# Performance work log

Measured on AMD Instinct MI355X. Metric: run time of the kernel, lower is better.

Reference implementation:

```python
import jax, jax.numpy as jnp
import numpy as np

EPS = 1e-10


def setup_inputs() -> dict:
    key = jax.random.key(0)
    k1, k2, k3 = jax.random.split(key, 3)
    B, c = 65536, 64
    xyz = jax.random.normal(k1, (B, 3, 1), dtype=jnp.float32)          # group centers
    xyz_group = xyz + 0.1 * jax.random.normal(k2, (B, 3, c), dtype=jnp.float32)  # neighbor points
    r_lrf = 0.2 + 0.8 * jax.random.uniform(k3, (B,), dtype=jnp.float32)  # per-group support radius
    return {"xyz": xyz, "xyz_group": xyz_group, "r_lrf": r_lrf}


def reference(xyz, xyz_group, r_lrf):
    # xyz: [B,3,1] center; xyz_group: [B,3,c] neighbors; r_lrf: [B]
    B, _, c = xyz_group.shape
    x = xyz - xyz_group                                   # [B,3,c]
    xxt = jnp.einsum('bic,bjc->bij', x, x) / c            # [B,3,3] covariance
    _, _, vh = jnp.linalg.svd(xxt)                        # vh: [B,3,3]
    v_last = vh[:, -1, :]                                 # [B,3] smallest singular vector (torch v[...,-1])

    # sign disambiguation (no-grad in the original)
    center_proj = jnp.einsum('bi,bic->bc', v_last, x)     # [B,c]
    sum_ = (center_proj > 0.001).sum(-1) - (center_proj < -0.001).sum(-1)  # [B]
    sign = jax.lax.stop_gradient(1.0 - 2.0 * (sum_ < 0).astype(jnp.float32))  # [B]

    zp = sign[:, None] * v_last                           # [B,3] z axis
    x = -x                                                # x *= -1 in original
    norm = jnp.einsum('bi,bic->bc', zp, x)                # [B,c] projection onto zp
    vi = x - zp[:, :, None] * norm[:, None, :]            # [B,3,c] in-plane component
    x_l2 = jnp.sqrt(jnp.sum(x * x, axis=1))               # [B,c]
    alpha = (r_lrf[:, None] - x_l2) ** 2                  # [B,c]
    beta = norm * norm                                    # [B,c]
    vi_c = jnp.einsum('bc,bic->bi', alpha * beta, vi)     # [B,3] weighted sum
    xp = vi_c / (jnp.sqrt(jnp.sum(vi_c * vi_c, axis=1, keepdims=True)) + EPS)  # [B,3] x axis
    yp = jnp.cross(xp, zp)                                # [B,3] y axis
    lrf = jnp.stack([xp, yp, zp], axis=2)                 # [B,3,3] columns = axes
    out = jnp.einsum('bij,bic->bjc', lrf, (xyz_group - xyz) / r_lrf[:, None, None])  # lrf^T @ _out_xp
    return out


if __name__ == '__main__':
    o = reference(**setup_inputs())
    print(o.shape)
```

## Files before the change

### kernel.cpp

```cpp
#include <hip/hip_runtime.h>


#define DEVFN static __device__ __forceinline__


DEVFN float slapy2f(float x, float y) {
#pragma clang fp contract(off)
  float xa = fabsf(x), ya = fabsf(y);
  float w = fmaxf(xa, ya);
  float z = fminf(xa, ya);
  if (z == 0.0f) return w;
  float q = z / w;
  return w * sqrtf(fmaf(q, q, 1.0f));
}

DEVFN float snrm2_2f(float a, float b) {
  double da = (double)a, db = (double)b;
  return (float)sqrt(da * da + db * db);
}

DEVFN void slartgf(float f, float g, float &cs, float &sn, float &r) {
#pragma clang fp contract(off)
  if (g == 0.0f) { cs = 1.0f; sn = 0.0f; r = f; return; }
  if (f == 0.0f) { cs = 0.0f; sn = copysignf(1.0f, g); r = fabsf(g); return; }
  float f1 = fabsf(f), g1 = fabsf(g);
  const float rtmin = 0x1p-63f;
  const float rtmax = 6.5219089e18f;
  if (f1 > rtmin && f1 < rtmax && g1 > rtmin && g1 < rtmax) {
    float d = sqrtf(fmaf(f, f, g * g));
    cs = f1 / d;
    r = copysignf(d, f);
    sn = g / r;
  } else {
    const float safmin = 0x1p-126f;
    const float safmax = 0x1p+126f;
    float u = fminf(safmax, fmaxf(safmin, fmaxf(f1, g1)));
    float fs = f / u, gs = g / u;
    float d = sqrtf(fmaf(fs, fs, gs * gs));
    cs = fabsf(fs) / d;
    r = copysignf(d, f);
    sn = gs / r;
    r = r * u;
  }
}

DEVFN void slas2f(float f, float g, float h, float &ssmin, float &ssmax) {
#pragma clang fp contract(off)
  float fa = fabsf(f), ga = fabsf(g), ha = fabsf(h);
  float fhmn = fminf(fa, ha), fhmx = fmaxf(fa, ha);
  if (fhmn == 0.0f) {
    ssmin = 0.0f;
    if (fhmx == 0.0f) {
      ssmax = ga;
    } else {
      float mx = fmaxf(fhmx, ga), mn = fminf(fhmx, ga);
      float q = mn / mx;
      ssmax = mx * sqrtf(fmaf(q, q, 1.0f));
    }
  } else {
    if (ga < fhmx) {
      float as = 1.0f + fhmn / fhmx;
      float at = (fhmx - fhmn) / fhmx;
      float qq = ga / fhmx;
      float au = qq * qq;
      float c = 2.0f / (sqrtf(fmaf(as, as, au)) + sqrtf(fmaf(at, at, au)));
      ssmin = fhmn * c;
      ssmax = fhmx / c;
    } else {
      float au = fhmx / ga;
      if (au == 0.0f) {
        ssmin = (fhmn * fhmx) / ga;
        ssmax = ga;
      } else {
        float as = 1.0f + fhmn / fhmx;
        float at = (fhmx - fhmn) / fhmx;
        float q1 = as * au, q2 = at * au;
        float c = 1.0f / (sqrtf(fmaf(q1, q1, 1.0f)) + sqrtf(fmaf(q2, q2, 1.0f)));
        ssmin = (fhmn * c) * au;
        ssmin = ssmin + ssmin;
        ssmax = ga / (c + c);
      }
    }
  }
}

DEVFN void slasv2f(float f, float g, float h, float &ssmin, float &ssmax,
                   float &snr, float &csr, float &snl, float &csl) {
#pragma clang fp contract(off)
  const float eps = 0x1p-24f;
  float ft = f, fa = fabsf(f), ht = h, ha = fabsf(h);
  int pmax = 1;
  bool swp = (ha > fa);
  if (swp) {
    pmax = 3;
    float tmp = ft; ft = ht; ht = tmp;
    tmp = fa; fa = ha; ha = tmp;
  }
  float gt = g, ga = fabsf(g);
  float clt = 0.0f, crt = 0.0f, slt = 0.0f, srt = 0.0f;
  if (ga == 0.0f) {
    ssmin = ha; ssmax = fa;
    clt = 1.0f; crt = 1.0f; slt = 0.0f; srt = 0.0f;
  } else {
    bool gasmal = true;
    if (ga > fa) {
      pmax = 2;
      if ((fa / ga) < eps) {
        gasmal = false;
        ssmax = ga;
        if (ha > 1.0f) ssmin = fa / (ga / ha);
        else ssmin = (fa / ga) * ha;
        clt = 1.0f; slt = ht / gt; srt = 1.0f; crt = ft / gt;
      }
    }
    if (gasmal) {
      float dd = fa - ha;
      float l;
      if (dd == fa) l = 1.0f;
      else l = dd / fa;
      float m = gt / ft;
      float t = 2.0f - l;
      float s = sqrtf(fmaf(m, m, t * t));
      float r;
      if (l == 0.0f) r = fabsf(m);
      else r = sqrtf(fmaf(m, m, l * l));
      float a = 0.5f * (s + r);
      ssmin = ha / a;
      ssmax = fa * a;
      float mm = m * m;
      if (mm == 0.0f) {
        if (l == 0.0f) t = copysignf(2.0f, ft) * copysignf(1.0f, gt);
        else t = gt / copysignf(dd, ft) + m / t;
      } else {
        t = (m / (s + t) + m / (r + l)) * (1.0f + a);
      }
      float l2 = sqrtf(fmaf(t, t, 4.0f));
      crt = 2.0f / l2;
      srt = t / l2;
      clt = fmaf(srt, m, crt) / a;
      slt = (ht / ft) * srt / a;
    }
  }
  if (swp) { csl = srt; snl = crt; csr = slt; snr = clt; }
  else { csl = clt; snl = slt; csr = crt; snr = srt; }
  float tsign = 0.0f;
  if (pmax == 1) tsign = copysignf(1.0f, csr) * copysignf(1.0f, csl) * copysignf(1.0f, f);
  if (pmax == 2) tsign = copysignf(1.0f, snr) * copysignf(1.0f, csl) * copysignf(1.0f, g);
  if (pmax == 3) tsign = copysignf(1.0f, snr) * copysignf(1.0f, snl) * copysignf(1.0f, h);
  ssmax = copysignf(ssmax, tsign);
  ssmin = copysignf(ssmin, tsign * copysignf(1.0f, f) * copysignf(1.0f, h));
}

#define GROT(hi1, hi2, hi3, lo1, lo2, lo3, ct_, st_)          \
  do {                                                        \
    float c__ = (ct_), s__ = (st_);                           \
    if (c__ != 1.0f || s__ != 0.0f) {                         \
      float t_;                                               \
      t_ = hi1; hi1 = fmaf(c__, t_, -(s__ * lo1)); lo1 = fmaf(s__, t_, c__ * lo1); \
      t_ = hi2; hi2 = fmaf(c__, t_, -(s__ * lo2)); lo2 = fmaf(s__, t_, c__ * lo2); \
      t_ = hi3; hi3 = fmaf(c__, t_, -(s__ * lo3)); lo3 = fmaf(s__, t_, c__ * lo3); \
    }                                                         \
  } while (0)

#define ROT2X2(lo1, lo2, lo3, hi1, hi2, hi3, cr_, sr_)        \
  do {                                                        \
    float xx_, yy_, st_;                                      \
    xx_ = lo1; yy_ = hi1; st_ = fmaf(cr_, xx_, sr_ * yy_);    \
    hi1 = fmaf(cr_, yy_, -(sr_ * xx_)); lo1 = st_;            \
    xx_ = lo2; yy_ = hi2; st_ = fmaf(cr_, xx_, sr_ * yy_);    \
    hi2 = fmaf(cr_, yy_, -(sr_ * xx_)); lo2 = st_;            \
    xx_ = lo3; yy_ = hi3; st_ = fmaf(cr_, xx_, sr_ * yy_);    \
    hi3 = fmaf(cr_, yy_, -(sr_ * xx_)); lo3 = st_;            \
  } while (0)

#define VSWAP(a, b) { float t_ = (a); (a) = (b); (b) = t_; }

static __device__ void svd3_vlast(float c00, float c01, float c02,
                                  float c11, float c12, float c22,
                                  float vout[3]) {
#pragma clang fp contract(off)
  float a11 = c00, a12 = c01, a13 = c02;
  float a21 = c01, a22 = c11, a23 = c12;
  float a31 = c02, a32 = c12, a33 = c22;
  float d1, d2, d3, e1, e2;
  float taup1 = 0.0f, g2 = 0.0f;

  {
    float xnorm = snrm2_2f(a21, a31);
    if (xnorm == 0.0f) {
      d1 = a11;
    } else {
      float beta = -copysignf(slapy2f(a11, xnorm), a11);
      float tauq1 = (beta - a11) / beta;
      float sc = 1.0f / (a11 - beta);
      float v2 = a21 * sc, v3 = a31 * sc;
      d1 = beta;
      float w2 = fmaf(a32, v3, a22 * v2);
      float w3 = fmaf(a33, v3, a23 * v2);
      w2 = w2 + a12;
      w3 = w3 + a13;
      a12 = fmaf(-tauq1, w2, a12);
      a13 = fmaf(-tauq1, w3, a13);
      float t2 = -tauq1 * w2;
      float t3 = -tauq1 * w3;
      a22 = fmaf(v2, t2, a22); a32 = fmaf(v3, t2, a32);
      a23 = fmaf(v2, t3, a23); a33 = fmaf(v3, t3, a33);
    }
  }
  {
    float xnorm = fabsf(a13);
    if (xnorm == 0.0f) {
      e1 = a12;
    } else {
      float beta = -copysignf(slapy2f(a12, xnorm), a12);
      taup1 = (beta - a12) / beta;
      g2 = a13 * (1.0f / (a12 - beta));
      e1 = beta;
      float w2 = a23 * g2;
      float w3 = a33 * g2;
      w2 = w2 + a22;
      w3 = w3 + a32;
      a22 = fmaf(-taup1, w2, a22);
      a32 = fmaf(-taup1, w3, a32);
      float tg = -taup1 * g2;
      a23 = fmaf(w2, tg, a23);
      a33 = fmaf(w3, tg, a33);
    }
  }
  {
    float xnorm = fabsf(a32);
    if (xnorm == 0.0f) {
      d2 = a22;
    } else {
      float beta = -copysignf(slapy2f(a22, xnorm), a22);
      float tauq2 = (beta - a22) / beta;
      float h3 = a32 * (1.0f / (a22 - beta));
      d2 = beta;
      float w = a33 * h3;
      w = w + a23;
      a23 = fmaf(-tauq2, w, a23);
      float tw = -tauq2 * w;
      a33 = fmaf(h3, tw, a33);
    }
  }
  e2 = a23;
  d3 = a33;

  float vt11 = 1.0f, vt12 = 0.0f, vt13 = 0.0f;
  float vt21 = 0.0f, vt22 = 1.0f, vt23 = 0.0f;
  float vt31 = 0.0f, vt32 = 0.0f, vt33 = 1.0f;

  const float eps = 0x1p-24f;
  const float unfl = 0x1p-126f;
  const float tol = 10.0f * eps;
  float thresh;
  {
    float sminoa = fabsf(d1);
    if (sminoa != 0.0f) {
      float mu = sminoa;
      mu = fabsf(d2) * (mu / (mu + fabsf(e1)));
      sminoa = fminf(sminoa, mu);
      if (sminoa != 0.0f) {
        mu = fabsf(d3) * (mu / (mu + fabsf(e2)));
        sminoa = fminf(sminoa, mu);
      }
    }
    sminoa = sminoa / sqrtf(3.0f);
    thresh = fmaxf(tol * sminoa, 6.0f * (3.0f * (3.0f * unfl)));
  }
  int mq = 3;
  int iterq = -1, iterdivn = 0;
  const int maxitdivn = 18;
  int oldll = -1, oldm = -1, idir = 0;
  float sminl = 0.0f;
  int guard = 0;

  while (true) {
    if (mq <= 1) break;
    if (++guard > 300) break;
    if (iterq >= 3) {
      iterq -= 3;
      iterdivn += 1;
      if (iterdivn >= maxitdivn) break;
    }
    if (mq == 2) {
      if (fabsf(e1) <= thresh) { e1 = 0.0f; mq = 1; continue; }
      float sigmn, sigmx, sinr, cosr, sinl, cosl;
      slasv2f(d1, e1, d2, sigmn, sigmx, sinr, cosr, sinl, cosl);
      d1 = sigmx; e1 = 0.0f; d2 = sigmn;
      ROT2X2(vt11, vt12, vt13, vt21, vt22, vt23, cosr, sinr);
      mq = 0;
      continue;
    }
    float smax = fabsf(d3);
    if (fabsf(e2) <= thresh) { e2 = 0.0f; mq = 2; continue; }
    smax = fmaxf(fmaxf(smax, fabsf(d2)), fabsf(e2));
    if (fabsf(e1) <= thresh) {
      e1 = 0.0f;
      float sigmn, sigmx, sinr, cosr, sinl, cosl;
      slasv2f(d2, e2, d3, sigmn, sigmx, sinr, cosr, sinl, cosl);
      d2 = sigmx; e2 = 0.0f; d3 = sigmn;
      ROT2X2(vt21, vt22, vt23, vt31, vt32, vt33, cosr, sinr);
      mq = 1;
      continue;
    }
    smax = fmaxf(fmaxf(smax, fabsf(d1)), fabsf(e1));
    if (1 > oldm || 3 < oldll)
      idir = (fabsf(d1) >= fabsf(d3)) ? 1 : 2;
    bool back = false;
    if (idir == 1) {
      if (fabsf(e2) <= tol * fabsf(d3)) { e2 = 0.0f; continue; }
      float mu = fabsf(d1);
      sminl = mu;
      if (fabsf(e1) <= tol * mu) { e1 = 0.0f; back = true; }
      else {
        mu = fabsf(d2) * (mu / (mu + fabsf(e1)));
        sminl = fminf(sminl, mu);
        if (fabsf(e2) <= tol * mu) { e2 = 0.0f; back = true; }
        else {
          mu = fabsf(d3) * (mu / (mu + fabsf(e2)));
          sminl = fminf(sminl, mu);
        }
      }
    } else {
      if (fabsf(e1) <= tol * fabsf(d1)) { e1 = 0.0f; continue; }
      float mu = fabsf(d3);
      sminl = mu;
      if (fabsf(e2) <= tol * mu) { e2 = 0.0f; back = true; }
      else {
        mu = fabsf(d2) * (mu / (mu + fabsf(e2)));
        sminl = fminf(sminl, mu);
        if (fabsf(e1) <= tol * mu) { e1 = 0.0f; back = true; }
        else {
          mu = fabsf(d1) * (mu / (mu + fabsf(e1)));
          sminl = fminf(sminl, mu);
        }
      }
    }
    if (back) continue;
    oldll = 1;
    oldm = 3;
    float shift = 0.0f;
    if (!((3.0f * tol) * (sminl / smax) <= fmaxf(eps, 0.01f * tol))) {
      float sll, rdum;
      if (idir == 1) { sll = fabsf(d1); slas2f(d2, e2, d3, shift, rdum); }
      else { sll = fabsf(d3); slas2f(d1, e1, d2, shift, rdum); }
      if (sll > 0.0f) {
        float q = shift / sll;
        if (q * q < eps) shift = 0.0f;
      }
    }
    iterq += 2;
    float rc0, rc1, rs0, rs1;
    if (shift == 0.0f) {
      if (idir == 1) {
        float cs = 1.0f, oldcs = 1.0f, sn = 0.0f, oldsn = 0.0f, rr = 0.0f;
        float fq = d1 * cs;
        slartgf(fq, e1, cs, sn, rr);
        float f2 = oldcs * rr;
        float g2q = d2 * sn;
        slartgf(f2, g2q, oldcs, oldsn, d1);
        rc0 = cs; rs0 = sn;
        fq = d2 * cs;
        slartgf(fq, e2, cs, sn, rr);
        e1 = oldsn * rr;
        f2 = oldcs * rr;
        g2q = d3 * sn;
        slartgf(f2, g2q, oldcs, oldsn, d2);
        rc1 = cs; rs1 = sn;
        float h = d3 * cs;
        d3 = h * oldcs;
        e2 = h * oldsn;
        GROT(vt21, vt22, vt23, vt11, vt12, vt13, rc0, rs0);
        GROT(vt31, vt32, vt33, vt21, vt22, vt23, rc1, rs1);
        if (fabsf(e2) <= thresh) e2 = 0.0f;
      } else {
        float cs = 1.0f, oldcs = 1.0f, sn = 0.0f, oldsn = 0.0f, rr = 0.0f;
        float fq = d3 * cs;
        slartgf(fq, e2, cs, sn, rr);
        float f2 = oldcs * rr;
        float g2q = d2 * sn;
        slartgf(f2, g2q, oldcs, oldsn, d3);
        rc1 = oldcs; rs1 = -oldsn;
        fq = d2 * cs;
        slartgf(fq, e1, cs, sn, rr);
        e2 = oldsn * rr;
        f2 = oldcs * rr;
        g2q = d1 * sn;
        slartgf(f2, g2q, oldcs, oldsn, d2);
        rc0 = oldcs; rs0 = -oldsn;
        float h = d1 * cs;
        d1 = h * oldcs;
        e1 = h * oldsn;
        GROT(vt31, vt32, vt33, vt21, vt22, vt23, rc1, rs1);
        GROT(vt21, vt22, vt23, vt11, vt12, vt13, rc0, rs0);
        if (fabsf(e1) <= thresh) e1 = 0.0f;
      }
    } else {
      if (idir == 1) {
        float fq = (fabsf(d1) - shift) * (copysignf(1.0f, d1) + shift / d1);
        float gq = e1;
        float cosr = 0, sinr = 0, cosl = 0, sinl = 0, rr = 0;
        slartgf(fq, gq, cosr, sinr, rr);
        fq = fmaf(cosr, d1, sinr * e1);
        e1 = fmaf(cosr, e1, -(sinr * d1));
        gq = sinr * d2;
        d2 = cosr * d2;
        slartgf(fq, gq, cosl, sinl, rr);
        d1 = rr;
        fq = fmaf(cosl, e1, sinl * d2);
        d2 = fmaf(cosl, d2, -(sinl * e1));
        gq = sinl * e2;
        e2 = cosl * e2;
        rc0 = cosr; rs0 = sinr;
        slartgf(fq, gq, cosr, sinr, rr);
        e1 = rr;
        fq = fmaf(cosr, d2, sinr * e2);
        e2 = fmaf(cosr, e2, -(sinr * d2));
        gq = sinr * d3;
        d3 = cosr * d3;
        slartgf(fq, gq, cosl, sinl, rr);
        d2 = rr;
        fq = fmaf(cosl, e2, sinl * d3);
        d3 = fmaf(cosl, d3, -(sinl * e2));
        rc1 = cosr; rs1 = sinr;
        e2 = fq;
        GROT(vt21, vt22, vt23, vt11, vt12, vt13, rc0, rs0);
        GROT(vt31, vt32, vt33, vt21, vt22, vt23, rc1, rs1);
        if (fabsf(e2) <= thresh) e2 = 0.0f;
      } else {
        float fq = (fabsf(d3) - shift) * (copysignf(1.0f, d3) + shift / d3);
        float gq = e2;
        float cosr = 0, sinr = 0, cosl = 0, sinl = 0, rr = 0;
        slartgf(fq, gq, cosr, sinr, rr);
        fq = fmaf(cosr, d3, sinr * e2);
        e2 = fmaf(cosr, e2, -(sinr * d3));
        gq = sinr * d2;
        d2 = cosr * d2;
        slartgf(fq, gq, cosl, sinl, rr);
        d3 = rr;
        fq = fmaf(cosl, e2, sinl * d2);
        d2 = fmaf(cosl, d2, -(sinl * e2));
        gq = sinl * e1;
        e1 = cosl * e1;
        rc1 = cosl; rs1 = -sinl;
        slartgf(fq, gq, cosr, sinr, rr);
        e2 = rr;
        fq = fmaf(cosr, d2, sinr * e1);
        e1 = fmaf(cosr, e1, -(sinr * d2));
        gq = sinr * d1;
        d1 = cosr * d1;
        slartgf(fq, gq, cosl, sinl, rr);
        d2 = rr;
        fq = fmaf(cosl, e1, sinl * d1);
        d1 = fmaf(cosl, d1, -(sinl * e1));
        rc0 = cosl; rs0 = -sinl;
        e1 = fq;
        if (fabsf(e1) <= thresh) e1 = 0.0f;
        GROT(vt31, vt32, vt33, vt21, vt22, vt23, rc1, rs1);
        GROT(vt21, vt22, vt23, vt11, vt12, vt13, rc0, rs0);
      }
    }
  }
  if (d1 < 0.0f) { d1 = -d1; vt11 = -vt11; vt12 = -vt12; vt13 = -vt13; }
  if (d2 < 0.0f) { d2 = -d2; vt21 = -vt21; vt22 = -vt22; vt23 = -vt23; }
  if (d3 < 0.0f) { d3 = -d3; vt31 = -vt31; vt32 = -vt32; vt33 = -vt33; }
  {
    int isub = 1; float smin = d1;
    if (d2 <= smin) { isub = 2; smin = d2; }
    if (d3 <= smin) { isub = 3; smin = d3; }
    if (isub != 3) {
      if (isub == 1) {
        d1 = d3; d3 = smin;
        VSWAP(vt11, vt31); VSWAP(vt12, vt32); VSWAP(vt13, vt33);
      } else {
        d2 = d3; d3 = smin;
        VSWAP(vt21, vt31); VSWAP(vt22, vt32); VSWAP(vt23, vt33);
      }
    }
  }
  {
    int isub = 1; float smin = d1;
    if (d2 <= smin) { isub = 2; smin = d2; }
    if (isub != 2) {
      d1 = d2; d2 = smin;
      VSWAP(vt11, vt21); VSWAP(vt12, vt22); VSWAP(vt13, vt23);
    }
  }
  float r1 = vt31, r2 = vt32, r3 = vt33;
  if (taup1 != 0.0f) {
    float w = r3 * g2;
    w = w + r2;
    r2 = fmaf(-taup1, w, r2);
    float tg = -taup1 * g2;
    r3 = fmaf(w, tg, r3);
  }
  vout[0] = r1;
  vout[1] = r2;
  vout[2] = r3;
}


#define JSWAP(a, b) { double t_ = (a); (a) = (b); (b) = t_; }

DEVFN void jacobi3(float c00f, float c01f, float c02f,
                   float c11f, float c12f, float c22f,
                   float vmin[3], float u2o[3], double &lmax, double &gap) {
  double a00 = (double)c00f, a01 = (double)c01f, a02 = (double)c02f;
  double a11 = (double)c11f, a12 = (double)c12f, a22 = (double)c22f;
  double v00 = 1.0, v01 = 0.0, v02 = 0.0;
  double v10 = 0.0, v11 = 1.0, v12 = 0.0;
  double v20 = 0.0, v21 = 0.0, v22 = 1.0;

#pragma unroll
  for (int sweep = 0; sweep < 4; ++sweep) {
    if (a01 != 0.0) {
      double tau = (a11 - a00) / (2.0 * a01);
      double t = (tau >= 0.0 ? 1.0 : -1.0) / (fabs(tau) + sqrt(1.0 + tau * tau));
      double c = 1.0 / sqrt(1.0 + t * t);
      double s = t * c;
      a00 = a00 - t * a01;
      a11 = a11 + t * a01;
      a01 = 0.0;
      double n02 = c * a02 - s * a12;
      double n12 = s * a02 + c * a12;
      a02 = n02; a12 = n12;
      double x;
      x = v00; v00 = c * x - s * v01; v01 = s * x + c * v01;
      x = v10; v10 = c * x - s * v11; v11 = s * x + c * v11;
      x = v20; v20 = c * x - s * v21; v21 = s * x + c * v21;
    }
    if (a02 != 0.0) {
      double tau = (a22 - a00) / (2.0 * a02);
      double t = (tau >= 0.0 ? 1.0 : -1.0) / (fabs(tau) + sqrt(1.0 + tau * tau));
      double c = 1.0 / sqrt(1.0 + t * t);
      double s = t * c;
      a00 = a00 - t * a02;
      a22 = a22 + t * a02;
      a02 = 0.0;
      double n01 = c * a01 - s * a12;
      double n12 = s * a01 + c * a12;
      a01 = n01; a12 = n12;
      double x;
      x = v00; v00 = c * x - s * v02; v02 = s * x + c * v02;
      x = v10; v10 = c * x - s * v12; v12 = s * x + c * v12;
      x = v20; v20 = c * x - s * v22; v22 = s * x + c * v22;
    }
    if (a12 != 0.0) {
      double tau = (a22 - a11) / (2.0 * a12);
      double t = (tau >= 0.0 ? 1.0 : -1.0) / (fabs(tau) + sqrt(1.0 + tau * tau));
      double c = 1.0 / sqrt(1.0 + t * t);
      double s = t * c;
      a11 = a11 - t * a12;
      a22 = a22 + t * a12;
      a12 = 0.0;
      double n01 = c * a01 - s * a02;
      double n02 = s * a01 + c * a02;
      a01 = n01; a02 = n02;
      double x;
      x = v01; v01 = c * x - s * v02; v02 = s * x + c * v02;
      x = v11; v11 = c * x - s * v12; v12 = s * x + c * v12;
      x = v21; v21 = c * x - s * v22; v22 = s * x + c * v22;
    }
  }

  double L0 = a00, L1 = a11, L2 = a22;
  if (L0 < L1) { JSWAP(L0, L1); JSWAP(v00, v01); JSWAP(v10, v11); JSWAP(v20, v21); }
  if (L0 < L2) { JSWAP(L0, L2); JSWAP(v00, v02); JSWAP(v10, v12); JSWAP(v20, v22); }
  if (L1 < L2) { JSWAP(L1, L2); JSWAP(v01, v02); JSWAP(v11, v12); JSWAP(v21, v22); }
  lmax = L0;
  gap = L1 - L2;

  double n2 = 1.0 / sqrt(v02 * v02 + v12 * v12 + v22 * v22);
  vmin[0] = (float)(v02 * n2);
  vmin[1] = (float)(v12 * n2);
  vmin[2] = (float)(v22 * n2);
  double n1 = 1.0 / sqrt(v01 * v01 + v11 * v11 + v21 * v21);
  u2o[0] = (float)(v01 * n1);
  u2o[1] = (float)(v11 * n1);
  u2o[2] = (float)(v21 * n1);
}

DEVFN float qsum(float x) {
#pragma clang fp contract(off)
  float s = x + __shfl_xor(x, 1);
  return s + __shfl_xor(s, 2);
}
DEVFN int qsumi(int x) {
  int s = x + __shfl_xor(x, 1);
  return s + __shfl_xor(s, 2);
}

#define CHAIN4(acc, A, Bv)            \
  do {                                \
    float t_ = A[3] * Bv[3] + acc;    \
    t_ = A[2] * Bv[2] + t_;           \
    t_ = A[1] * Bv[1] + t_;           \
    acc = A[0] * Bv[0] + t_;          \
  } while (0)

#define PASS3(Z0, Z1, Z2, OVX, OVY, OVZ)                      \
  do {                                                        \
    float vx = 0, vy = 0, vz = 0;                             \
    _Pragma("unroll")                                         \
    for (int Bk = 0; Bk < 4; ++Bk) {                          \
      float w[4], q0[4], q1[4], q2[4];                        \
      _Pragma("unroll")                                       \
      for (int j = 0; j < 4; ++j) {                           \
        int i = 4 * Bk + j;                                   \
        float y0 = r0[i] - cx;                                \
        float y1 = r1[i] - cy;                                \
        float y2 = r2[i] - cz;                                \
        float nm = (Z0) * y0;                                 \
        nm = (Z1) * y1 + nm;                                  \
        nm = (Z2) * y2 + nm;                                  \
        q0[j] = y0 - (Z0) * nm;                               \
        q1[j] = y1 - (Z1) * nm;                               \
        q2[j] = y2 - (Z2) * nm;                               \
        float ss_ = y0 * y0;                                  \
        ss_ = ss_ + y1 * y1;                                  \
        ss_ = ss_ + y2 * y2;                                  \
        float xl2_ = sqrtf(ss_);                              \
        float am_ = r - xl2_;                                 \
        float alpha_ = am_ * am_;                             \
        float beta_ = nm * nm;                                \
        w[j] = alpha_ * beta_;                                \
      }                                                       \
      CHAIN4(vx, w, q0);                                      \
      CHAIN4(vy, w, q1);                                      \
      CHAIN4(vz, w, q2);                                      \
    }                                                         \
    OVX = qsum(vx);                                           \
    OVY = qsum(vy);                                           \
    OVZ = qsum(vz);                                           \
  } while (0)


__global__ __launch_bounds__(256)
__attribute__((amdgpu_waves_per_eu(2, 4)))
void LRF_70695161692718_main(
    const float* __restrict__ xyz, const float* __restrict__ xyzg,
    const float* __restrict__ rl, float* __restrict__ out,
    float* __restrict__ ws, int B) {
#pragma clang fp contract(off)
  int tid = blockIdx.x * blockDim.x + threadIdx.x;
  int b = tid >> 2;
  int l = tid & 3;
  if (b >= B) return;
  const float* Xg = xyzg + (size_t)b * 192;
  float cx = xyz[3 * b + 0], cy = xyz[3 * b + 1], cz = xyz[3 * b + 2];
  float r = rl[b];

  float r0[16], r1[16], r2[16];
#pragma unroll
  for (int i = 0; i < 16; ++i) {
    int col = 4 * i + l;
    r0[i] = Xg[col];
    r1[i] = Xg[64 + col];
    r2[i] = Xg[128 + col];
  }

  float a00 = 0, a01 = 0, a02 = 0, a11 = 0, a12 = 0, a22 = 0;
#pragma unroll
  for (int Bk = 0; Bk < 4; ++Bk) {
    float x0[4], x1[4], x2[4];
#pragma unroll
    for (int j = 0; j < 4; ++j) {
      int i = 4 * Bk + j;
      x0[j] = cx - r0[i];
      x1[j] = cy - r1[i];
      x2[j] = cz - r2[i];
    }
    CHAIN4(a00, x0, x0);
    CHAIN4(a01, x0, x1);
    CHAIN4(a02, x0, x2);
    CHAIN4(a11, x1, x1);
    CHAIN4(a12, x1, x2);
    CHAIN4(a22, x2, x2);
  }
  a00 = qsum(a00) / 64.0f;
  a01 = qsum(a01) / 64.0f;
  a02 = qsum(a02) / 64.0f;
  a11 = qsum(a11) / 64.0f;
  a12 = qsum(a12) / 64.0f;
  a22 = qsum(a22) / 64.0f;

  float v[3], u2[3];
  double lmax, gap;
  jacobi3(a00, a01, a02, a11, a12, a22, v, u2, lmax, gap);

  int flag = !(gap > 0.032 * lmax);

  const float MARG = 3.1e-5f;
  int npos = 0, nneg = 0, nshk = 0;
#pragma unroll
  for (int i = 0; i < 16; ++i) {
    float x0 = cx - r0[i];
    float x1 = cy - r1[i];
    float x2 = cz - r2[i];
    float p = v[0] * x0;
    p = v[1] * x1 + p;
    p = v[2] * x2 + p;
    float ss_ = x0 * x0;
    ss_ = ss_ + x1 * x1;
    ss_ = ss_ + x2 * x2;
    float xl2_ = sqrtf(ss_);
    npos += (p > 0.001f) ? 1 : 0;
    nneg += (p < -0.001f) ? 1 : 0;
    nshk += (fabsf(fabsf(p) - 0.001f) <= MARG * xl2_) ? 1 : 0;
  }
  int sum_ = qsumi(npos) - qsumi(nneg);
  int nsh = qsumi(nshk);
  flag |= (sum_ >= -nsh) && (sum_ <= nsh);

  float sgn = (sum_ < 0) ? -1.0f : 1.0f;
  float zp0 = sgn * v[0], zp1 = sgn * v[1], zp2 = sgn * v[2];

  float vcx, vcy, vcz;
  PASS3(zp0, zp1, zp2, vcx, vcy, vcz);
  float pz0 = sgn * (v[0] + 3e-5f * u2[0]);
  float pz1 = sgn * (v[1] + 3e-5f * u2[1]);
  float pz2 = sgn * (v[2] + 3e-5f * u2[2]);
  float wcx, wcy, wcz;
  PASS3(pz0, pz1, pz2, wcx, wcy, wcz);

  float ss = vcx * vcx;
  ss = ss + vcy * vcy;
  ss = ss + vcz * vcz;
  float vnorm = sqrtf(ss);
  float den = vnorm + 1e-10f;
  float xp0 = vcx / den, xp1 = vcy / den, xp2 = vcz / den;

  float ssp = wcx * wcx + wcy * wcy + wcz * wcz;
  float denp = sqrtf(ssp) + 1e-10f;
  float qp0 = wcx / denp, qp1 = wcy / denp, qp2 = wcz / denp;
  float d0 = xp0 - qp0, d1 = xp1 - qp1, d2 = xp2 - qp2;
  float d2sum = d0 * d0 + d1 * d1 + d2 * d2;
  float dv0 = vcx - wcx, dv1 = vcy - wcy, dv2 = vcz - wcz;
  float dvic2 = dv0 * dv0 + dv1 * dv1 + dv2 * dv2;
  flag |= !(d2sum < 1.2e-5f);
  flag |= !(vnorm * vnorm > 900.0f * dvic2);

  float yp0 = xp1 * zp2 - xp2 * zp1;
  float yp1 = xp2 * zp0 - xp0 * zp2;
  float yp2 = xp0 * zp1 - xp1 * zp0;

  float* O = out + (size_t)b * 192;
#pragma unroll
  for (int i = 0; i < 16; ++i) {
    int col = 4 * i + l;
    float y0 = r0[i] - cx;
    float y1 = r1[i] - cy;
    float y2 = r2[i] - cz;
    float p0 = y0 / r, p1 = y1 / r, p2 = y2 / r;
    float t0 = xp0 * p0; t0 = xp1 * p1 + t0; t0 = xp2 * p2 + t0;
    float t1 = yp0 * p0; t1 = yp1 * p1 + t1; t1 = yp2 * p2 + t1;
    float t2 = zp0 * p0; t2 = zp1 * p1 + t2; t2 = zp2 * p2 + t2;
    O[col] = t0;
    O[64 + col] = t1;
    O[128 + col] = t2;
  }

  if (l == 0) {
    float* s = ws + (size_t)b * 8;
    s[0] = flag ? 1.0f : 0.0f;
    if (flag) {
      s[1] = a00; s[2] = a01; s[3] = a02;
      s[4] = a11; s[5] = a12; s[6] = a22;
    }
  }
}


__global__ __launch_bounds__(256)
__attribute__((amdgpu_waves_per_eu(2, 4)))
void LRF_70695161692718_fix(
    const float* __restrict__ xyz, const float* __restrict__ xyzg,
    const float* __restrict__ rl, float* __restrict__ out,
    const float* __restrict__ ws, int B) {
#pragma clang fp contract(off)
  int tid = blockIdx.x * blockDim.x + threadIdx.x;
  int b = tid >> 2;
  int l = tid & 3;
  if (b >= B) return;
  const float* s = ws + (size_t)b * 8;
  if (s[0] == 0.0f) return;

  float a00 = s[1], a01 = s[2], a02 = s[3];
  float a11 = s[4], a12 = s[5], a22 = s[6];

  float v[3];
  svd3_vlast(a00, a01, a02, a11, a12, a22, v);

  const float* Xg = xyzg + (size_t)b * 192;
  float cx = xyz[3 * b + 0], cy = xyz[3 * b + 1], cz = xyz[3 * b + 2];
  float r = rl[b];

  float r0[16], r1[16], r2[16];
#pragma unroll
  for (int i = 0; i < 16; ++i) {
    int col = 4 * i + l;
    r0[i] = Xg[col];
    r1[i] = Xg[64 + col];
    r2[i] = Xg[128 + col];
  }

  int npos = 0, nneg = 0;
#pragma unroll
  for (int i = 0; i < 16; ++i) {
    float x0 = cx - r0[i];
    float x1 = cy - r1[i];
    float x2 = cz - r2[i];
    float p = v[0] * x0;
    p = v[1] * x1 + p;
    p = v[2] * x2 + p;
    npos += (p > 0.001f) ? 1 : 0;
    nneg += (p < -0.001f) ? 1 : 0;
  }
  int sum_ = qsumi(npos) - qsumi(nneg);
  float sgn = (sum_ < 0) ? -1.0f : 1.0f;
  float zp0 = sgn * v[0], zp1 = sgn * v[1], zp2 = sgn * v[2];

  float vcx, vcy, vcz;
  PASS3(zp0, zp1, zp2, vcx, vcy, vcz);
  float ss = vcx * vcx;
  ss = ss + vcy * vcy;
  ss = ss + vcz * vcz;
  float den = sqrtf(ss) + 1e-10f;
  float xp0 = vcx / den, xp1 = vcy / den, xp2 = vcz / den;
  float yp0 = xp1 * zp2 - xp2 * zp1;
  float yp1 = xp2 * zp0 - xp0 * zp2;
  float yp2 = xp0 * zp1 - xp1 * zp0;

  float* O = out + (size_t)b * 192;
#pragma unroll
  for (int i = 0; i < 16; ++i) {
    int col = 4 * i + l;
    float y0 = r0[i] - cx;
    float y1 = r1[i] - cy;
    float y2 = r2[i] - cz;
    float p0 = y0 / r, p1 = y1 / r, p2 = y2 / r;
    float t0 = xp0 * p0; t0 = xp1 * p1 + t0; t0 = xp2 * p2 + t0;
    float t1 = yp0 * p0; t1 = yp1 * p1 + t1; t1 = yp2 * p2 + t1;
    float t2 = zp0 * p0; t2 = zp1 * p1 + t2; t2 = zp2 * p2 + t2;
    O[col] = t0;
    O[64 + col] = t1;
    O[128 + col] = t2;
  }
}


__global__ __launch_bounds__(256)
__attribute__((amdgpu_waves_per_eu(2, 4)))
void LRF_70695161692718_mono(
    const float* __restrict__ xyz, const float* __restrict__ xyzg,
    const float* __restrict__ rl, float* __restrict__ out, int B) {
#pragma clang fp contract(off)
  int tid = blockIdx.x * blockDim.x + threadIdx.x;
  int b = tid >> 2;
  int l = tid & 3;
  if (b >= B) return;
  const float* Xg = xyzg + (size_t)b * 192;
  float cx = xyz[3 * b + 0], cy = xyz[3 * b + 1], cz = xyz[3 * b + 2];
  float r = rl[b];

  float r0[16], r1[16], r2[16];
#pragma unroll
  for (int i = 0; i < 16; ++i) {
    int col = 4 * i + l;
    r0[i] = Xg[col];
    r1[i] = Xg[64 + col];
    r2[i] = Xg[128 + col];
  }

  float a00 = 0, a01 = 0, a02 = 0, a11 = 0, a12 = 0, a22 = 0;
#pragma unroll
  for (int Bk = 0; Bk < 4; ++Bk) {
    float x0[4], x1[4], x2[4];
#pragma unroll
    for (int j = 0; j < 4; ++j) {
      int i = 4 * Bk + j;
      x0[j] = cx - r0[i];
      x1[j] = cy - r1[i];
      x2[j] = cz - r2[i];
    }
    CHAIN4(a00, x0, x0);
    CHAIN4(a01, x0, x1);
    CHAIN4(a02, x0, x2);
    CHAIN4(a11, x1, x1);
    CHAIN4(a12, x1, x2);
    CHAIN4(a22, x2, x2);
  }
  a00 = qsum(a00) / 64.0f;
  a01 = qsum(a01) / 64.0f;
  a02 = qsum(a02) / 64.0f;
  a11 = qsum(a11) / 64.0f;
  a12 = qsum(a12) / 64.0f;
  a22 = qsum(a22) / 64.0f;

  float v[3];
  svd3_vlast(a00, a01, a02, a11, a12, a22, v);

  int npos = 0, nneg = 0;
#pragma unroll
  for (int i = 0; i < 16; ++i) {
    float x0 = cx - r0[i];
    float x1 = cy - r1[i];
    float x2 = cz - r2[i];
    float p = v[0] * x0;
    p = v[1] * x1 + p;
    p = v[2] * x2 + p;
    npos += (p > 0.001f) ? 1 : 0;
    nneg += (p < -0.001f) ? 1 : 0;
  }
  int sum_ = qsumi(npos) - qsumi(nneg);
  float sgn = (sum_ < 0) ? -1.0f : 1.0f;
  float zp0 = sgn * v[0], zp1 = sgn * v[1], zp2 = sgn * v[2];

  float vcx, vcy, vcz;
  PASS3(zp0, zp1, zp2, vcx, vcy, vcz);
  float ss = vcx * vcx;
  ss = ss + vcy * vcy;
  ss = ss + vcz * vcz;
  float den = sqrtf(ss) + 1e-10f;
  float xp0 = vcx / den, xp1 = vcy / den, xp2 = vcz / den;
  float yp0 = xp1 * zp2 - xp2 * zp1;
  float yp1 = xp2 * zp0 - xp0 * zp2;
  float yp2 = xp0 * zp1 - xp1 * zp0;

  float* O = out + (size_t)b * 192;
#pragma unroll
  for (int i = 0; i < 16; ++i) {
    int col = 4 * i + l;
    float y0 = r0[i] - cx;
    float y1 = r1[i] - cy;
    float y2 = r2[i] - cz;
    float p0 = y0 / r, p1 = y1 / r, p2 = y2 / r;
    float t0 = xp0 * p0; t0 = xp1 * p1 + t0; t0 = xp2 * p2 + t0;
    float t1 = yp0 * p0; t1 = yp1 * p1 + t1; t1 = yp2 * p2 + t1;
    float t2 = zp0 * p0; t2 = zp1 * p1 + t2; t2 = zp2 * p2 + t2;
    O[col] = t0;
    O[64 + col] = t1;
    O[128 + col] = t2;
  }
}

extern "C" void kernel_launch(void* const* d_in, const int* in_sizes, int n_in,
                              void* d_out, int out_size, void* d_ws, size_t ws_size,
                              hipStream_t stream) {
  (void)n_in; (void)out_size;
  const float* xyz = (const float*)d_in[0];
  const float* xyzg = (const float*)d_in[1];
  const float* rl = (const float*)d_in[2];
  float* out = (float*)d_out;
  int B = in_sizes[2];
  int blocks = (B * 4 + 255) / 256;

  if (d_ws != nullptr && ws_size >= (size_t)B * 32) {
    float* ws = (float*)d_ws;
    LRF_70695161692718_main<<<blocks, 256, 0, stream>>>(xyz, xyzg, rl, out, ws, B);
    LRF_70695161692718_fix<<<blocks, 256, 0, stream>>>(xyz, xyzg, rl, out, ws, B);
  } else {
    LRF_70695161692718_mono<<<blocks, 256, 0, stream>>>(xyz, xyzg, rl, out, B);
  }
}
```

Before: 177.0 us.

## Use float Jacobi, single-pass sensitivity check, and compacted fixup worklist

The fast-path Jacobi eigensolver moves from double to float with more sweeps, and the second perturbed PASS3 reduction is replaced by an analytic sensitivity bound accumulated in the same pass. The sqrt in the sign-margin test becomes a squared comparison. Flagged groups are now pushed to a compact list through an atomic counter, so the fix kernel only launches work for those groups instead of scanning every group's flag. This cuts FP64 work and one full data pass, but the float solver and the new heuristic bound risk misflagging groups, and an unused jacobi3f function is left behind.

```diff
diff --git a/kernel.cpp b/kernel.cpp
--- a/kernel.cpp
+++ b/kernel.cpp
@@ -501,84 +501,155 @@
 }
 
 
-#define JSWAP(a, b) { double t_ = (a); (a) = (b); (b) = t_; }
-
-DEVFN void jacobi3(float c00f, float c01f, float c02f,
-                   float c11f, float c12f, float c22f,
-                   float vmin[3], float u2o[3], double &lmax, double &gap) {
-  double a00 = (double)c00f, a01 = (double)c01f, a02 = (double)c02f;
-  double a11 = (double)c11f, a12 = (double)c12f, a22 = (double)c22f;
-  double v00 = 1.0, v01 = 0.0, v02 = 0.0;
-  double v10 = 0.0, v11 = 1.0, v12 = 0.0;
-  double v20 = 0.0, v21 = 0.0, v22 = 1.0;
-
-#pragma unroll
-  for (int sweep = 0; sweep < 4; ++sweep) {
-    if (a01 != 0.0) {
-      double tau = (a11 - a00) / (2.0 * a01);
-      double t = (tau >= 0.0 ? 1.0 : -1.0) / (fabs(tau) + sqrt(1.0 + tau * tau));
-      double c = 1.0 / sqrt(1.0 + t * t);
-      double s = t * c;
+#define JSWAPF(a, b) { float t_ = (a); (a) = (b); (b) = t_; }
+
+DEVFN void jacobi3f(float a00, float a01, float a02,
+                    float a11, float a12, float a22,
+                    float vmin[3], float &lmax, float &gap) {
+  float v00 = 1.0f, v01 = 0.0f, v02 = 0.0f;
+  float v10 = 0.0f, v11 = 1.0f, v12 = 0.0f;
+  float v20 = 0.0f, v21 = 0.0f, v22 = 1.0f;
+
+#pragma unroll
+  for (int sweep = 0; sweep < 6; ++sweep) {
+    if (a01 != 0.0f) {
+      float tau = (a11 - a00) / (2.0f * a01);
+      float t = (tau >= 0.0f ? 1.0f : -1.0f) / (fabsf(tau) + sqrtf(fmaf(tau, tau, 1.0f)));
+      float c = 1.0f / sqrtf(fmaf(t, t, 1.0f));
+      float s = t * c;
       a00 = a00 - t * a01;
       a11 = a11 + t * a01;
-      a01 = 0.0;
-      double n02 = c * a02 - s * a12;
-      double n12 = s * a02 + c * a12;
+      a01 = 0.0f;
+      float n02 = c * a02 - s * a12;
+      float n12 = s * a02 + c * a12;
       a02 = n02; a12 = n12;
-      double x;
+      float x;
       x = v00; v00 = c * x - s * v01; v01 = s * x + c * v01;
       x = v10; v10 = c * x - s * v11; v11 = s * x + c * v11;
       x = v20; v20 = c * x - s * v21; v21 = s * x + c * v21;
     }
-    if (a02 != 0.0) {
-      double tau = (a22 - a00) / (2.0 * a02);
-      double t = (tau >= 0.0 ? 1.0 : -1.0) / (fabs(tau) + sqrt(1.0 + tau * tau));
-      double c = 1.0 / sqrt(1.0 + t * t);
-      double s = t * c;
+    if (a02 != 0.0f) {
+      float tau = (a22 - a00) / (2.0f * a02);
+      float t = (tau >= 0.0f ? 1.0f : -1.0f) / (fabsf(tau) + sqrtf(fmaf(tau, tau, 1.0f)));
+      float c = 1.0f / sqrtf(fmaf(t, t, 1.0f));
+      float s = t * c;
       a00 = a00 - t * a02;
       a22 = a22 + t * a02;
-      a02 = 0.0;
-      double n01 = c * a01 - s * a12;
-      double n12 = s * a01 + c * a12;
+      a02 = 0.0f;
+      float n01 = c * a01 - s * a12;
+      float n12 = s * a01 + c * a12;
       a01 = n01; a12 = n12;
-      double x;
+      float x;
       x = v00; v00 = c * x - s * v02; v02 = s * x + c * v02;
       x = v10; v10 = c * x - s * v12; v12 = s * x + c * v12;
       x = v20; v20 = c * x - s * v22; v22 = s * x + c * v22;
     }
-    if (a12 != 0.0) {
-      double tau = (a22 - a11) / (2.0 * a12);
-      double t = (tau >= 0.0 ? 1.0 : -1.0) / (fabs(tau) + sqrt(1.0 + tau * tau));
-      double c = 1.0 / sqrt(1.0 + t * t);
-      double s = t * c;
+    if (a12 != 0.0f) {
+      float tau = (a22 - a11) / (2.0f * a12);
+      float t = (tau >= 0.0f ? 1.0f : -1.0f) / (fabsf(tau) + sqrtf(fmaf(tau, tau, 1.0f)));
+      float c = 1.0f / sqrtf(fmaf(t, t, 1.0f));
+      float s = t * c;
       a11 = a11 - t * a12;
+      a12 = 0.0f;
       a22 = a22 + t * a12;
-      a12 = 0.0;
-      double n01 = c * a01 - s * a02;
-      double n02 = s * a01 + c * a02;
-      a01 = n01; a02 = n02;
-      double x;
+      float x;
       x = v01; v01 = c * x - s * v02; v02 = s * x + c * v02;
       x = v11; v11 = c * x - s * v12; v12 = s * x + c * v12;
       x = v21; v21 = c * x - s * v22; v22 = s * x + c * v22;
-    }
-  }
-
-  double L0 = a00, L1 = a11, L2 = a22;
-  if (L0 < L1) { JSWAP(L0, L1); JSWAP(v00, v01); JSWAP(v10, v11); JSWAP(v20, v21); }
-  if (L0 < L2) { JSWAP(L0, L2); JSWAP(v00, v02); JSWAP(v10, v12); JSWAP(v20, v22); }
-  if (L1 < L2) { JSWAP(L1, L2); JSWAP(v01, v02); JSWAP(v11, v12); JSWAP(v21, v22); }
+      float n01 = c * a01 - s * a02;
+      float n02 = s * a01 + c * a02;
+      a01 = n01; a02 = n02;
+      (void)0;
+    }
+  }
+
+
+  float L0 = a00, L1 = a11, L2 = a22;
+  if (L0 < L1) { JSWAPF(L0, L1); JSWAPF(v00, v01); JSWAPF(v10, v11); JSWAPF(v20, v21); }
+  if (L0 < L2) { JSWAPF(L0, L2); JSWAPF(v00, v02); JSWAPF(v10, v12); JSWAPF(v20, v22); }
+  if (L1 < L2) { JSWAPF(L1, L2); JSWAPF(v01, v02); JSWAPF(v11, v12); JSWAPF(v21, v22); }
   lmax = L0;
   gap = L1 - L2;
 
-  double n2 = 1.0 / sqrt(v02 * v02 + v12 * v12 + v22 * v22);
-  vmin[0] = (float)(v02 * n2);
-  vmin[1] = (float)(v12 * n2);
-  vmin[2] = (float)(v22 * n2);
-  double n1 = 1.0 / sqrt(v01 * v01 + v11 * v11 + v21 * v21);
-  u2o[0] = (float)(v01 * n1);
-  u2o[1] = (float)(v11 * n1);
-  u2o[2] = (float)(v21 * n1);
+  float n2 = 1.0f / sqrtf(v02 * v02 + v12 * v12 + v22 * v22);
+  vmin[0] = v02 * n2;
+  vmin[1] = v12 * n2;
+  vmin[2] = v22 * n2;
+}
+
+DEVFN void jacobi3f_fixed(float a00, float a01, float a02,
+                          float a11, float a12, float a22,
+                          float vmin[3], float &lmax, float &gap) {
+  float v00 = 1.0f, v01 = 0.0f, v02 = 0.0f;
+  float v10 = 0.0f, v11 = 1.0f, v12 = 0.0f;
+  float v20 = 0.0f, v21 = 0.0f, v22 = 1.0f;
+
+#pragma unroll
+  for (int sweep = 0; sweep < 6; ++sweep) {
+    if (a01 != 0.0f) {
+      float tau = (a11 - a00) / (2.0f * a01);
+      float t = (tau >= 0.0f ? 1.0f : -1.0f) / (fabsf(tau) + sqrtf(fmaf(tau, tau, 1.0f)));
+      float c = 1.0f / sqrtf(fmaf(t, t, 1.0f));
+      float s = t * c;
+      float old01 = a01;
+      a00 = a00 - t * old01;
+      a11 = a11 + t * old01;
+      a01 = 0.0f;
+      float n02 = c * a02 - s * a12;
+      float n12 = s * a02 + c * a12;
+      a02 = n02; a12 = n12;
+      float x;
+      x = v00; v00 = c * x - s * v01; v01 = s * x + c * v01;
+      x = v10; v10 = c * x - s * v11; v11 = s * x + c * v11;
+      x = v20; v20 = c * x - s * v21; v21 = s * x + c * v21;
+    }
+    if (a02 != 0.0f) {
+      float tau = (a22 - a00) / (2.0f * a02);
+      float t = (tau >= 0.0f ? 1.0f : -1.0f) / (fabsf(tau) + sqrtf(fmaf(tau, tau, 1.0f)));
+      float c = 1.0f / sqrtf(fmaf(t, t, 1.0f));
+      float s = t * c;
+      float old02 = a02;
+      a00 = a00 - t * old02;
+      a22 = a22 + t * old02;
+      a02 = 0.0f;
+      float n01 = c * a01 - s * a12;
+      float n12 = s * a01 + c * a12;
+      a01 = n01; a12 = n12;
+      float x;
+      x = v00; v00 = c * x - s * v02; v02 = s * x + c * v02;
+      x = v10; v10 = c * x - s * v12; v12 = s * x + c * v12;
+      x = v20; v20 = c * x - s * v22; v22 = s * x + c * v22;
+    }
+    if (a12 != 0.0f) {
+      float tau = (a22 - a11) / (2.0f * a12);
+      float t = (tau >= 0.0f ? 1.0f : -1.0f) / (fabsf(tau) + sqrtf(fmaf(tau, tau, 1.0f)));
+      float c = 1.0f / sqrtf(fmaf(t, t, 1.0f));
+      float s = t * c;
+      float old12 = a12;
+      a11 = a11 - t * old12;
+      a22 = a22 + t * old12;
+      a12 = 0.0f;
+      float n01 = c * a01 - s * a02;
+      float n02 = s * a01 + c * a02;
+      a01 = n01; a02 = n02;
+      float x;
+      x = v01; v01 = c * x - s * v02; v02 = s * x + c * v02;
+      x = v11; v11 = c * x - s * v12; v12 = s * x + c * v12;
+      x = v21; v21 = c * x - s * v22; v22 = s * x + c * v22;
+    }
+  }
+
+  float L0 = a00, L1 = a11, L2 = a22;
+  if (L0 < L1) { JSWAPF(L0, L1); JSWAPF(v00, v01); JSWAPF(v10, v11); JSWAPF(v20, v21); }
+  if (L0 < L2) { JSWAPF(L0, L2); JSWAPF(v00, v02); JSWAPF(v10, v12); JSWAPF(v20, v22); }
+  if (L1 < L2) { JSWAPF(L1, L2); JSWAPF(v01, v02); JSWAPF(v11, v12); JSWAPF(v21, v22); }
+  lmax = L0;
+  gap = L1 - L2;
+
+  float n2 = 1.0f / sqrtf(v02 * v02 + v12 * v12 + v22 * v22);
+  vmin[0] = v02 * n2;
+  vmin[1] = v12 * n2;
+  vmin[2] = v22 * n2;
 }
 
 DEVFN float qsum(float x) {
@@ -641,7 +712,8 @@
 void LRF_70695161692718_main(
     const float* __restrict__ xyz, const float* __restrict__ xyzg,
     const float* __restrict__ rl, float* __restrict__ out,
-    float* __restrict__ ws, int B) {
+    float* __restrict__ covws, int* __restrict__ cnt, int* __restrict__ list,
+    int B) {
 #pragma clang fp contract(off)
   int tid = blockIdx.x * blockDim.x + threadIdx.x;
   int b = tid >> 2;
@@ -685,13 +757,13 @@
   a12 = qsum(a12) / 64.0f;
   a22 = qsum(a22) / 64.0f;
 
-  float v[3], u2[3];
-  double lmax, gap;
-  jacobi3(a00, a01, a02, a11, a12, a22, v, u2, lmax, gap);
-
-  int flag = !(gap > 0.032 * lmax);
-
-  const float MARG = 3.1e-5f;
+  float v[3];
+  float lmax, gap;
+  jacobi3f_fixed(a00, a01, a02, a11, a12, a22, v, lmax, gap);
+
+  int flag = !(gap > 0.032f * lmax);
+
+  const float MARG2 = 9.61e-10f;
   int npos = 0, nneg = 0, nshk = 0;
 #pragma unroll
   for (int i = 0; i < 16; ++i) {
@@ -704,10 +776,10 @@
     float ss_ = x0 * x0;
     ss_ = ss_ + x1 * x1;
     ss_ = ss_ + x2 * x2;
-    float xl2_ = sqrtf(ss_);
+    float d = fabsf(fabsf(p) - 0.001f);
     npos += (p > 0.001f) ? 1 : 0;
     nneg += (p < -0.001f) ? 1 : 0;
-    nshk += (fabsf(fabsf(p) - 0.001f) <= MARG * xl2_) ? 1 : 0;
+    nshk += (d * d <= MARG2 * ss_) ? 1 : 0;
   }
   int sum_ = qsumi(npos) - qsumi(nneg);
   int nsh = qsumi(nshk);
@@ -716,13 +788,40 @@
   float sgn = (sum_ < 0) ? -1.0f : 1.0f;
   float zp0 = sgn * v[0], zp1 = sgn * v[1], zp2 = sgn * v[2];
 
-  float vcx, vcy, vcz;
-  PASS3(zp0, zp1, zp2, vcx, vcy, vcz);
-  float pz0 = sgn * (v[0] + 3e-5f * u2[0]);
-  float pz1 = sgn * (v[1] + 3e-5f * u2[1]);
-  float pz2 = sgn * (v[2] + 3e-5f * u2[2]);
-  float wcx, wcy, wcz;
-  PASS3(pz0, pz1, pz2, wcx, wcy, wcz);
+  float vx = 0, vy = 0, vz = 0, ssen = 0;
+#pragma unroll
+  for (int Bk = 0; Bk < 4; ++Bk) {
+    float w[4], q0[4], q1[4], q2[4];
+#pragma unroll
+    for (int j = 0; j < 4; ++j) {
+      int i = 4 * Bk + j;
+      float y0 = r0[i] - cx;
+      float y1 = r1[i] - cy;
+      float y2 = r2[i] - cz;
+      float nm = zp0 * y0;
+      nm = zp1 * y1 + nm;
+      nm = zp2 * y2 + nm;
+      q0[j] = y0 - zp0 * nm;
+      q1[j] = y1 - zp1 * nm;
+      q2[j] = y2 - zp2 * nm;
+      float ss_ = y0 * y0;
+      ss_ = ss_ + y1 * y1;
+      ss_ = ss_ + y2 * y2;
+      float xl2_ = sqrtf(ss_);
+      float am_ = r - xl2_;
+      float alpha_ = am_ * am_;
+      float beta_ = nm * nm;
+      w[j] = alpha_ * beta_;
+      ssen += alpha_ * fabsf(nm) * ss_;
+    }
+    CHAIN4(vx, w, q0);
+    CHAIN4(vy, w, q1);
+    CHAIN4(vz, w, q2);
+  }
+  float vcx = qsum(vx);
+  float vcy = qsum(vy);
+  float vcz = qsum(vz);
+  float SS = qsum(ssen);
 
   float ss = vcx * vcx;
   ss = ss + vcy * vcy;
@@ -731,19 +830,22 @@
   float den = vnorm + 1e-10f;
   float xp0 = vcx / den, xp1 = vcy / den, xp2 = vcz / den;
 
-  float ssp = wcx * wcx + wcy * wcy + wcz * wcz;
-  float denp = sqrtf(ssp) + 1e-10f;
-  float qp0 = wcx / denp, qp1 = wcy / denp, qp2 = wcz / denp;
-  float d0 = xp0 - qp0, d1 = xp1 - qp1, d2 = xp2 - qp2;
-  float d2sum = d0 * d0 + d1 * d1 + d2 * d2;
-  float dv0 = vcx - wcx, dv1 = vcy - wcy, dv2 = vcz - wcz;
-  float dvic2 = dv0 * dv0 + dv1 * dv1 + dv2 * dv2;
-  flag |= !(d2sum < 1.2e-5f);
-  flag |= !(vnorm * vnorm > 900.0f * dvic2);
+  flag |= !(1.2e-4f * SS < 1.75e-3f * vnorm);
 
   float yp0 = xp1 * zp2 - xp2 * zp1;
   float yp1 = xp2 * zp0 - xp0 * zp2;
   float yp2 = xp0 * zp1 - xp1 * zp0;
+
+  if (flag) {
+    if (l == 0) {
+      float* s = covws + (size_t)b * 6;
+      s[0] = a00; s[1] = a01; s[2] = a02;
+      s[3] = a11; s[4] = a12; s[5] = a22;
+      int pos = atomicAdd(cnt, 1);
+      list[pos] = b;
+    }
+    return;
+  }
 
   float* O = out + (size_t)b * 192;
 #pragma unroll
@@ -760,15 +862,6 @@
     O[64 + col] = t1;
     O[128 + col] = t2;
   }
-
-  if (l == 0) {
-    float* s = ws + (size_t)b * 8;
-    s[0] = flag ? 1.0f : 0.0f;
-    if (flag) {
-      s[1] = a00; s[2] = a01; s[3] = a02;
-      s[4] = a11; s[5] = a12; s[6] = a22;
-    }
-  }
 }
 
 
@@ -777,17 +870,19 @@
 void LRF_70695161692718_fix(
     const float* __restrict__ xyz, const float* __restrict__ xyzg,
     const float* __restrict__ rl, float* __restrict__ out,
-    const float* __restrict__ ws, int B) {
+    const float* __restrict__ covws, const int* __restrict__ cnt,
+    const int* __restrict__ list, int B) {
 #pragma clang fp contract(off)
   int tid = blockIdx.x * blockDim.x + threadIdx.x;
-  int b = tid >> 2;
+  int idx = tid >> 2;
   int l = tid & 3;
-  if (b >= B) return;
-  const float* s = ws + (size_t)b * 8;
-  if (s[0] == 0.0f) return;
-
-  float a00 = s[1], a01 = s[2], a02 = s[3];
-  float a11 = s[4], a12 = s[5], a22 = s[6];
+  int n = *cnt;
+  if (idx >= n) return;
+  int b = list[idx];
+
+  const float* s = covws + (size_t)b * 6;
+  float a00 = s[0], a01 = s[1], a02 = s[2];
+  float a11 = s[3], a12 = s[4], a22 = s[5];
 
   float v[3];
   svd3_vlast(a00, a01, a02, a11, a12, a22, v);
@@ -956,10 +1051,16 @@
   int B = in_sizes[2];
   int blocks = (B * 4 + 255) / 256;
 
-  if (d_ws != nullptr && ws_size >= (size_t)B * 32) {
-    float* ws = (float*)d_ws;
-    LRF_70695161692718_main<<<blocks, 256, 0, stream>>>(xyz, xyzg, rl, out, ws, B);
-    LRF_70695161692718_fix<<<blocks, 256, 0, stream>>>(xyz, xyzg, rl, out, ws, B);
+  size_t need = (size_t)B * 24 + 64 + (size_t)B * 4;
+  if (d_ws != nullptr && ws_size >= need) {
+    float* covws = (float*)d_ws;
+    int* cnt = (int*)((char*)d_ws + (size_t)B * 24);
+    int* list = cnt + 16;
+    hipMemsetAsync(cnt, 0, 4, stream);
+    LRF_70695161692718_main<<<blocks, 256, 0, stream>>>(
+        xyz, xyzg, rl, out, covws, cnt, list, B);
+    LRF_70695161692718_fix<<<blocks, 256, 0, stream>>>(
+        xyz, xyzg, rl, out, covws, cnt, list, B);
   } else {
     LRF_70695161692718_mono<<<blocks, 256, 0, stream>>>(xyz, xyzg, rl, out, B);
   }
```

Result: slower. 186.5 us (+5.3%).
